# Optimization experiments

Measured on AMD Instinct MI355X. Metric: run time of the kernel, lower is better.

Reference implementation:

```python
import jax, jax.numpy as jnp
import numpy as np

B, NH, T, N, D = 4, 8, 2048, 512, 128
THETA = 2.0 ** 16
GAMMA = 0.995


def setup_inputs() -> dict:
    key = jax.random.key(0)
    kq, kv, ks = jax.random.split(key, 3)
    Q = jax.random.normal(kq, (B, NH, T, N), jnp.float32)
    V = jax.random.normal(kv, (B, NH, T, D), jnp.float32)
    S_prev = 0.01 * jax.random.normal(ks, (B, NH, N, D), jnp.float32)
    # get_freqs(N, theta=2**16): per-channel inverse frequencies
    freqs = jnp.asarray(1.0 / THETA ** (np.arange(N, dtype=np.float32) / N), jnp.float32)
    gamma = jnp.float32(GAMMA)
    return {"Q": Q, "V": V, "S_prev": S_prev, "freqs": freqs, "gamma": gamma}


def _rope(phases, v):
    """Rotary embedding with per-channel phases. phases broadcasts against v's
    last two dims (T, N); rotate-half formulation."""
    cos, sin = jnp.cos(phases), jnp.sin(phases)
    half = v.shape[-1] // 2
    v_rot = jnp.concatenate([-v[..., half:], v[..., :half]], axis=-1)
    return v * cos + v_rot * sin


def reference(Q, V, S_prev, freqs, gamma):
    # Q: (B,nh,T,N)  V: (B,nh,T,D)  S_prev: (B,nh,N,D)
    t_len = Q.shape[2]
    phases = jnp.arange(t_len, dtype=freqs.dtype)[:, None] * freqs[None, :]  # (T,N)
    QR = _rope(phases[None, None], Q)  # K == Q per the module's assert

    q_seq = jnp.moveaxis(QR, 2, 0)  # (T,B,nh,N)
    v_seq = jnp.moveaxis(V, 2, 0)   # (T,B,nh,D)

    def step(S, qv):
        q_t, v_t = qv
        out_t = jnp.einsum('bhn,bhnd->bhd', q_t, S)          # read before write
        S_new = (S + jnp.einsum('bhn,bhd->bhnd', q_t, v_t)) * gamma  # write + decay
        return S_new, out_t

    S_final, outs = jax.lax.scan(step, S_prev, (q_seq, v_seq))
    output = jnp.moveaxis(outs, 0, 2)  # (B,nh,T,D)
    return output, S_final
```

## Files before the change

kernel.cpp:

```cpp
#include <hip/hip_runtime.h>
#include <hip/hip_bf16.h>

typedef __attribute__((ext_vector_type(8))) short short8;
typedef __attribute__((ext_vector_type(4))) float f32x4;

#define MFMA16(a,b,c) __builtin_amdgcn_mfma_f32_16x16x32_bf16((a),(b),(c),0,0,0)

constexpr int BHn = 32;
constexpr int Tn  = 2048;
constexpr int Nn  = 512;
constexpr int Dn  = 128;
constexpr int CHn = 64;
constexpr int NCH = Tn / CHn;

static __device__ __forceinline__ unsigned short f2b(float x){
  __hip_bfloat16 h = __float2bfloat16(x);
  return *reinterpret_cast<unsigned short*>(&h);
}

__global__ __launch_bounds__(256) void rope_k(const float* __restrict__ Q,
                                              const float* __restrict__ freqs,
                                              unsigned short* __restrict__ QR){
  int gid = blockIdx.x * 256 + threadIdx.x;
  int np  = gid & 255;
  int t   = gid >> 8;
  float tf = (float)t;
  float f1 = freqs[np], f2 = freqs[np + 256];
  float s1, c1, s2, c2;
  sincosf(tf * f1, &s1, &c1);
  sincosf(tf * f2, &s2, &c2);
  size_t off = (size_t)t * Nn + np;
  for (int bh = 0; bh < BHn; ++bh){
    size_t base = (size_t)bh * Tn * Nn + off;
    float q1 = Q[base], q2 = Q[base + 256];
    QR[base]       = f2b(q1 * c1 - q2 * s1);
    QR[base + 256] = f2b(q2 * c2 + q1 * s2);
  }
}

__device__ __forceinline__ short8 ldfrag(const unsigned short* buf, int rowbase, int k0, int ld, int lane){
  int row = rowbase + (lane & 15);
  int col = (k0 + ((lane >> 4) << 3)) ^ ((row & 7) << 3);
  return *reinterpret_cast<const short8*>(buf + row * ld + col);
}
__device__ __forceinline__ short8 gfrag(const unsigned short* Qc, int rowbase, int k0, int lane){
  return *reinterpret_cast<const short8*>(
      Qc + (size_t)(rowbase + (lane & 15)) * Nn + k0 + ((lane >> 4) << 3));
}
__device__ __forceinline__ void stage_Rs(unsigned short* Rs, uint4 a, uint4 b, int dt, int n0){
  *reinterpret_cast<uint4*>(&Rs[ dt      * 512 + (n0 ^ (( dt      & 7) << 3))]) = a;
  *reinterpret_cast<uint4*>(&Rs[(dt + 1) * 512 + (n0 ^ (((dt + 1) & 7) << 3))]) = b;
}

__global__ __launch_bounds__(256) void pt_k(const unsigned short* __restrict__ QR,
                                            const float* __restrict__ gammap,
                                            unsigned short* __restrict__ Pt){
  __shared__ __align__(16) unsigned short Rs[64 * 512];
  __shared__ float gpow[65];
  const int tid = threadIdx.x, w = tid >> 6, lane = tid & 63;
  const int bh = blockIdx.x & 31, c = blockIdx.x >> 5;
  if (tid < 65) gpow[tid] = powf(gammap[0], (float)tid);
  const unsigned short* Qc = QR + (size_t)bh * Tn * Nn + (size_t)(c * CHn) * Nn;
  #pragma unroll
  for (int i = 0; i < 8; ++i){
    int p  = tid + i * 256;
    int dt = (p >> 6) << 1, n0 = (p & 63) << 3;
    const unsigned short* src = Qc + (size_t)dt * Nn + n0;
    uint4 a = *reinterpret_cast<const uint4*>(src);
    uint4 b = *reinterpret_cast<const uint4*>(src + Nn);
    stage_Rs(Rs, a, b, dt, n0);
  }
  __syncthreads();
  f32x4 p0 = {0.f,0.f,0.f,0.f}, p1 = p0, p2 = p0;
  for (int kb = 0; kb < 16; ++kb){
    int k0 = kb * 32;
    if (w == 0){
      short8 f0 = ldfrag(Rs,  0, k0, 512, lane);
      short8 f1 = ldfrag(Rs, 16, k0, 512, lane);
      p0 = MFMA16(f0, f0, p0);
      p1 = MFMA16(f1, f0, p1);
      p2 = MFMA16(f1, f1, p2);
    } else if (w == 1){
      short8 f0 = ldfrag(Rs,  0, k0, 512, lane);
      short8 f1 = ldfrag(Rs, 16, k0, 512, lane);
      short8 f2 = ldfrag(Rs, 32, k0, 512, lane);
      p0 = MFMA16(f2, f0, p0);
      p1 = MFMA16(f2, f1, p1);
      p2 = MFMA16(f2, f2, p2);
    } else if (w == 2){
      short8 f0 = ldfrag(Rs,  0, k0, 512, lane);
      short8 f1 = ldfrag(Rs, 16, k0, 512, lane);
      short8 f3 = ldfrag(Rs, 48, k0, 512, lane);
      p0 = MFMA16(f3, f0, p0);
      p1 = MFMA16(f3, f1, p1);
    } else {
      short8 f2 = ldfrag(Rs, 32, k0, 512, lane);
      short8 f3 = ldfrag(Rs, 48, k0, 512, lane);
      p0 = MFMA16(f3, f2, p0);
      p1 = MFMA16(f3, f3, p1);
    }
  }
  unsigned short* Pq = Pt + (size_t)(bh * NCH + c) * 4096;
  auto pwrite = [&](f32x4 pa, int tI, int tJ){
    int j  = tJ * 16 + (lane & 15);
    int i0 = tI * 16 + ((lane >> 4) << 2);
    #pragma unroll
    for (int r = 0; r < 4; ++r){
      int i = i0 + r;
      float v = (j < i) ? pa[r] * gpow[i] : 0.f;
      Pq[i * 64 + (j ^ ((i & 7) << 3))] = f2b(v);
    }
  };
  if      (w == 0){ pwrite(p0,0,0); pwrite(p1,1,0); pwrite(p2,1,1); pwrite(p0,0,1); }
  else if (w == 1){ pwrite(p0,2,0); pwrite(p1,2,1); pwrite(p2,2,2); pwrite(p0,0,2); }
  else if (w == 2){ pwrite(p0,3,0); pwrite(p1,3,1); pwrite(p0,0,3); pwrite(p1,1,2); }
  else            { pwrite(p0,3,2); pwrite(p1,3,3); pwrite(p0,1,3); pwrite(p1,2,3); }
}

__global__ __launch_bounds__(512, 1) void lattn_main(
    const unsigned short* __restrict__ QR,
    const unsigned short* __restrict__ Pt,
    const float* __restrict__ V,
    const float* __restrict__ S_prev,
    const float* __restrict__ gammap,
    float* __restrict__ Out,
    float* __restrict__ Sfin)
{
  __shared__ __align__(16) unsigned short SbTs[16 * 512];
  __shared__ __align__(16) unsigned short VTs[2][16 * 64];
  __shared__ float gpow[65], gpinv[65];

  const int tid  = threadIdx.x;
  const int w    = tid >> 6;
  const int lane = tid & 63;
  const int bh   = blockIdx.x & 31;
  const int dch  = blockIdx.x >> 5;
  const int d0   = dch * 16;
  const float g  = gammap[0];

  const unsigned short* QRbh = QR + (size_t)bh * Tn * Nn;
  const unsigned short* Ptbh = Pt + (size_t)bh * NCH * 4096;
  const float* Vbh = V + (size_t)bh * Tn * Dn;

  if (tid < 65){
    gpow[tid]  = powf(g,  (float)tid);
    gpinv[tid] = powf(g, -(float)tid);
  }

  const int snt = (w < 4) ? 2 : 6;
  const int sb  = (w < 4) ? w * 2 : 8 + (w - 4) * 6;
  f32x4 st[6];
  #pragma unroll
  for (int j = 0; j < 6; ++j) if (j < snt){
    int n = (sb + j) * 16 + (lane & 15);
    st[j] = *reinterpret_cast<const f32x4*>(
        S_prev + (size_t)bh * Nn * Dn + (size_t)n * Dn + d0 + ((lane >> 4) << 2));
  }
  __syncthreads();
  const float g64 = gpow[64];

  #pragma unroll
  for (int j = 0; j < 6; ++j) if (j < snt){
    int n  = (sb + j) * 16 + (lane & 15);
    int dl = (lane >> 4) << 2;
    #pragma unroll
    for (int r = 0; r < 4; ++r){
      int d = dl + r;
      SbTs[d * 512 + (n ^ ((d & 7) << 3))] = f2b(st[j][r]);
    }
  }
  {
    int dtv = tid >> 3, dp = (tid & 7) << 1;
    const float* vp = Vbh + (size_t)dtv * Dn + d0 + dp;
    float sc = gpinv[dtv];
    VTs[0][ dp      * 64 + (dtv ^ (( dp      & 7) << 3))] = f2b(vp[0] * sc);
    VTs[0][(dp + 1) * 64 + (dtv ^ (((dp + 1) & 7) << 3))] = f2b(vp[1] * sc);
  }
  __syncthreads();

  for (int c = 0; c < NCH; ++c){
    const int t0 = c * CHn;
    const int vb = c & 1;
    const bool pf = (c + 1 < NCH);
    const unsigned short* Qc = QRbh + (size_t)t0 * Nn;

    float va0 = 0.f, va1 = 0.f;
    const int dtv_ = tid >> 3;
    if (pf){
      const float* vp = Vbh + (size_t)(t0 + CHn + dtv_) * Dn + d0 + ((tid & 7) << 1);
      va0 = vp[0]; va1 = vp[1];
    }

    if (w < 4){
      f32x4 oacc = {0.f, 0.f, 0.f, 0.f};
      for (int kb = 0; kb < 16; ++kb){
        int k0 = kb * 32;
        short8 fs = ldfrag(SbTs, 0, k0, 512, lane);
        short8 fi = gfrag(Qc, w * 16, k0, lane);
        oacc = MFMA16(fs, fi, oacc);
      }
      float gi = gpow[w * 16 + (lane & 15)];
      #pragma unroll
      for (int r = 0; r < 4; ++r) oacc[r] *= gi;
      const unsigned short* Pq = Ptbh + (size_t)c * 4096;
      #pragma unroll
      for (int ks = 0; ks < 2; ++ks){
        short8 av = ldfrag(VTs[vb], 0, ks * 32, 64, lane);
        short8 bp = ldfrag(Pq, w * 16, ks * 32, 64, lane);
        oacc = MFMA16(av, bp, oacc);
      }
      int ti = t0 + w * 16 + (lane & 15);
      *reinterpret_cast<f32x4*>(
          Out + (size_t)bh * Tn * Dn + (size_t)ti * Dn + d0 + ((lane >> 4) << 2)) = oacc;
    }
    #pragma unroll
    for (int ks = 0; ks < 2; ++ks){
      short8 av = ldfrag(VTs[vb], 0, ks * 32, 64, lane);
      #pragma unroll
      for (int j = 0; j < 6; ++j) if (j < snt){
        int n = (sb + j) * 16 + (lane & 15);
        const unsigned short* col = Qc + (size_t)(ks * 32 + ((lane >> 4) << 3)) * Nn + n;
        short8 bn;
        #pragma unroll
        for (int e = 0; e < 8; ++e) bn[e] = (short)col[(size_t)e * Nn];
        st[j] = MFMA16(av, bn, st[j]);
      }
    }
    #pragma unroll
    for (int j = 0; j < 6; ++j) if (j < snt)
      #pragma unroll
      for (int r = 0; r < 4; ++r) st[j][r] *= g64;
    __syncthreads();

    #pragma unroll
    for (int j = 0; j < 6; ++j) if (j < snt){
      int n  = (sb + j) * 16 + (lane & 15);
      int dl = (lane >> 4) << 2;
      #pragma unroll
      for (int r = 0; r < 4; ++r){
        int d = dl + r;
        SbTs[d * 512 + (n ^ ((d & 7) << 3))] = f2b(st[j][r]);
      }
    }
    if (pf){
      int dp = (tid & 7) << 1;
      float sc = gpinv[dtv_];
      VTs[vb ^ 1][ dp      * 64 + (dtv_ ^ (( dp      & 7) << 3))] = f2b(va0 * sc);
      VTs[vb ^ 1][(dp + 1) * 64 + (dtv_ ^ (((dp + 1) & 7) << 3))] = f2b(va1 * sc);
    }
    __syncthreads();
  }

  #pragma unroll
  for (int j = 0; j < 6; ++j) if (j < snt){
    int n = (sb + j) * 16 + (lane & 15);
    *reinterpret_cast<f32x4*>(
        Sfin + (size_t)bh * Nn * Dn + (size_t)n * Dn + d0 + ((lane >> 4) << 2)) = st[j];
  }
}

extern "C" void kernel_launch(void* const* d_in, const int* in_sizes, int n_in,
                              void* d_out, int out_size, void* d_ws, size_t ws_size,
                              hipStream_t stream){
  const float* Q      = (const float*)d_in[0];
  const float* V      = (const float*)d_in[1];
  const float* S_prev = (const float*)d_in[2];
  const float* freqs  = (const float*)d_in[3];
  const float* gamma  = (const float*)d_in[4];
  float* Out  = (float*)d_out;
  float* Sfin = Out + (size_t)BHn * Tn * Dn;
  unsigned short* QR = (unsigned short*)d_ws;
  unsigned short* Pt = QR + (size_t)BHn * Tn * Nn;

  rope_k<<<2048, 256, 0, stream>>>(Q, freqs, QR);
  pt_k<<<1024, 256, 0, stream>>>(QR, gamma, Pt);
  lattn_main<<<256, 512, 0, stream>>>(QR, Pt, V, S_prev, gamma, Out, Sfin);
}
```

Baseline: 225.0 us.

## Double chunk length to 128 and add off-diagonal intra-chunk P kernel

Raises the chunk size of the chunked linear-attention recurrence from 64 to 128, halving the number of sequential state-update iterations and barriers in the main kernel. The intra-chunk P matrix becomes 128x128. It is built from two diagonal 64-blocks by the existing pt_k and a new po_k kernel for the off-diagonal block. V staging now uses vectorized float4 loads. The trade-off is more intra-chunk work and larger decay exponents (gamma^-127 scaling in bf16), which may affect accuracy.

```diff
diff --git a/kernel.cpp b/kernel.cpp
--- a/kernel.cpp
+++ b/kernel.cpp
@@ -10,7 +10,7 @@
 constexpr int Tn  = 2048;
 constexpr int Nn  = 512;
 constexpr int Dn  = 128;
-constexpr int CHn = 64;
+constexpr int CHn = 128;
 constexpr int NCH = Tn / CHn;
 
 static __device__ __forceinline__ unsigned short f2b(float x){
@@ -56,11 +56,12 @@
                                             const float* __restrict__ gammap,
                                             unsigned short* __restrict__ Pt){
   __shared__ __align__(16) unsigned short Rs[64 * 512];
-  __shared__ float gpow[65];
+  __shared__ float gpow[129];
   const int tid = threadIdx.x, w = tid >> 6, lane = tid & 63;
-  const int bh = blockIdx.x & 31, c = blockIdx.x >> 5;
-  if (tid < 65) gpow[tid] = powf(gammap[0], (float)tid);
-  const unsigned short* Qc = QR + (size_t)bh * Tn * Nn + (size_t)(c * CHn) * Nn;
+  const int bh = blockIdx.x & 31, cc = (blockIdx.x >> 5) & 15, sub = blockIdx.x >> 9;
+  const int ro = sub * 64;
+  if (tid < 129) gpow[tid] = powf(gammap[0], (float)tid);
+  const unsigned short* Qc = QR + (size_t)bh * Tn * Nn + (size_t)(cc * CHn + ro) * Nn;
   #pragma unroll
   for (int i = 0; i < 8; ++i){
     int p  = tid + i * 256;
@@ -100,21 +101,55 @@
       p1 = MFMA16(f3, f3, p1);
     }
   }
-  unsigned short* Pq = Pt + (size_t)(bh * NCH + c) * 4096;
+  unsigned short* Pq = Pt + (size_t)(bh * NCH + cc) * (CHn * CHn);
   auto pwrite = [&](f32x4 pa, int tI, int tJ){
     int j  = tJ * 16 + (lane & 15);
     int i0 = tI * 16 + ((lane >> 4) << 2);
     #pragma unroll
     for (int r = 0; r < 4; ++r){
       int i = i0 + r;
-      float v = (j < i) ? pa[r] * gpow[i] : 0.f;
-      Pq[i * 64 + (j ^ ((i & 7) << 3))] = f2b(v);
+      float v = (j < i) ? pa[r] * gpow[i + ro] : 0.f;
+      Pq[(i + ro) * CHn + ro + (j ^ ((i & 7) << 3))] = f2b(v);
     }
   };
   if      (w == 0){ pwrite(p0,0,0); pwrite(p1,1,0); pwrite(p2,1,1); pwrite(p0,0,1); }
   else if (w == 1){ pwrite(p0,2,0); pwrite(p1,2,1); pwrite(p2,2,2); pwrite(p0,0,2); }
   else if (w == 2){ pwrite(p0,3,0); pwrite(p1,3,1); pwrite(p0,0,3); pwrite(p1,1,2); }
   else            { pwrite(p0,3,2); pwrite(p1,3,3); pwrite(p0,1,3); pwrite(p1,2,3); }
+}
+
+__global__ __launch_bounds__(256) void po_k(const unsigned short* __restrict__ QR,
+                                            const float* __restrict__ gammap,
+                                            unsigned short* __restrict__ Pt){
+  __shared__ float gpow[129];
+  const int tid = threadIdx.x, w = tid >> 6, lane = tid & 63;
+  const int bh = blockIdx.x & 31, cc = blockIdx.x >> 5;
+  if (tid < 129) gpow[tid] = powf(gammap[0], (float)tid);
+  __syncthreads();
+  const unsigned short* QB = QR + (size_t)bh * Tn * Nn + (size_t)(cc * CHn) * Nn;
+  const unsigned short* QA = QB + (size_t)64 * Nn;
+  f32x4 acc[4] = {{0.f,0.f,0.f,0.f},{0.f,0.f,0.f,0.f},{0.f,0.f,0.f,0.f},{0.f,0.f,0.f,0.f}};
+  for (int kb = 0; kb < 16; ++kb){
+    int k0 = kb * 32;
+    short8 fa = gfrag(QA, w * 16, k0, lane);
+    #pragma unroll
+    for (int t = 0; t < 4; ++t){
+      short8 fb = gfrag(QB, t * 16, k0, lane);
+      acc[t] = MFMA16(fa, fb, acc[t]);
+    }
+  }
+  unsigned short* Pq = Pt + (size_t)(bh * NCH + cc) * (CHn * CHn);
+  #pragma unroll
+  for (int t = 0; t < 4; ++t){
+    int j  = t * 16 + (lane & 15);
+    int i0 = w * 16 + ((lane >> 4) << 2);
+    #pragma unroll
+    for (int r = 0; r < 4; ++r){
+      int i = i0 + r;
+      float v = acc[t][r] * gpow[64 + i];
+      Pq[(64 + i) * CHn + (j ^ ((i & 7) << 3))] = f2b(v);
+    }
+  }
 }
 
 __global__ __launch_bounds__(512, 1) void lattn_main(
@@ -127,8 +162,8 @@
     float* __restrict__ Sfin)
 {
   __shared__ __align__(16) unsigned short SbTs[16 * 512];
-  __shared__ __align__(16) unsigned short VTs[2][16 * 64];
-  __shared__ float gpow[65], gpinv[65];
+  __shared__ __align__(16) unsigned short VTs[2][16 * 128];
+  __shared__ float gpow[129], gpinv[129];
 
   const int tid  = threadIdx.x;
   const int w    = tid >> 6;
@@ -139,10 +174,10 @@
   const float g  = gammap[0];
 
   const unsigned short* QRbh = QR + (size_t)bh * Tn * Nn;
-  const unsigned short* Ptbh = Pt + (size_t)bh * NCH * 4096;
+  const unsigned short* Ptbh = Pt + (size_t)bh * NCH * (CHn * CHn);
   const float* Vbh = V + (size_t)bh * Tn * Dn;
 
-  if (tid < 65){
+  if (tid < 129){
     gpow[tid]  = powf(g,  (float)tid);
     gpinv[tid] = powf(g, -(float)tid);
   }
@@ -157,7 +192,7 @@
         S_prev + (size_t)bh * Nn * Dn + (size_t)n * Dn + d0 + ((lane >> 4) << 2));
   }
   __syncthreads();
-  const float g64 = gpow[64];
+  const float g128 = gpow[128];
 
   #pragma unroll
   for (int j = 0; j < 6; ++j) if (j < snt){
@@ -170,11 +205,14 @@
     }
   }
   {
-    int dtv = tid >> 3, dp = (tid & 7) << 1;
-    const float* vp = Vbh + (size_t)dtv * Dn + d0 + dp;
+    int dtv = tid >> 2, dp0 = (tid & 3) << 2;
+    f32x4 v4 = *reinterpret_cast<const f32x4*>(Vbh + (size_t)dtv * Dn + d0 + dp0);
     float sc = gpinv[dtv];
-    VTs[0][ dp      * 64 + (dtv ^ (( dp      & 7) << 3))] = f2b(vp[0] * sc);
-    VTs[0][(dp + 1) * 64 + (dtv ^ (((dp + 1) & 7) << 3))] = f2b(vp[1] * sc);
+    #pragma unroll
+    for (int r = 0; r < 4; ++r){
+      int d = dp0 + r;
+      VTs[0][d * 128 + (dtv ^ ((d & 7) << 3))] = f2b(v4[r] * sc);
+    }
   }
   __syncthreads();
 
@@ -184,38 +222,47 @@
     const bool pf = (c + 1 < NCH);
     const unsigned short* Qc = QRbh + (size_t)t0 * Nn;
 
-    float va0 = 0.f, va1 = 0.f;
-    const int dtv_ = tid >> 3;
-    if (pf){
-      const float* vp = Vbh + (size_t)(t0 + CHn + dtv_) * Dn + d0 + ((tid & 7) << 1);
-      va0 = vp[0]; va1 = vp[1];
-    }
+    f32x4 va4 = {0.f, 0.f, 0.f, 0.f};
+    const int dtv_ = tid >> 2, dp0_ = (tid & 3) << 2;
+    if (pf)
+      va4 = *reinterpret_cast<const f32x4*>(Vbh + (size_t)(t0 + CHn + dtv_) * Dn + d0 + dp0_);
 
     if (w < 4){
-      f32x4 oacc = {0.f, 0.f, 0.f, 0.f};
+      const int it0 = w, it1 = w + 4;
+      f32x4 o0 = {0.f,0.f,0.f,0.f}, o1 = o0;
       for (int kb = 0; kb < 16; ++kb){
         int k0 = kb * 32;
         short8 fs = ldfrag(SbTs, 0, k0, 512, lane);
-        short8 fi = gfrag(Qc, w * 16, k0, lane);
-        oacc = MFMA16(fs, fi, oacc);
-      }
-      float gi = gpow[w * 16 + (lane & 15)];
-      #pragma unroll
-      for (int r = 0; r < 4; ++r) oacc[r] *= gi;
-      const unsigned short* Pq = Ptbh + (size_t)c * 4096;
-      #pragma unroll
-      for (int ks = 0; ks < 2; ++ks){
-        short8 av = ldfrag(VTs[vb], 0, ks * 32, 64, lane);
-        short8 bp = ldfrag(Pq, w * 16, ks * 32, 64, lane);
-        oacc = MFMA16(av, bp, oacc);
-      }
-      int ti = t0 + w * 16 + (lane & 15);
+        short8 fa = gfrag(Qc, it0 * 16, k0, lane);
+        short8 fb = gfrag(Qc, it1 * 16, k0, lane);
+        o0 = MFMA16(fs, fa, o0);
+        o1 = MFMA16(fs, fb, o1);
+      }
+      float g0 = gpow[it0 * 16 + (lane & 15)];
+      float g1 = gpow[it1 * 16 + (lane & 15)];
+      #pragma unroll
+      for (int r = 0; r < 4; ++r){ o0[r] *= g0; o1[r] *= g1; }
+      const unsigned short* Pq = Ptbh + (size_t)c * (CHn * CHn);
+      #pragma unroll
+      for (int ks = 0; ks < 4; ++ks){
+        short8 av = ldfrag(VTs[vb], 0, ks * 32, 128, lane);
+        if (ks < 2){
+          short8 b0 = ldfrag(Pq, it0 * 16, ks * 32, CHn, lane);
+          o0 = MFMA16(av, b0, o0);
+        }
+        short8 b1 = ldfrag(Pq, it1 * 16, ks * 32, CHn, lane);
+        o1 = MFMA16(av, b1, o1);
+      }
+      int ti0 = t0 + it0 * 16 + (lane & 15);
+      int ti1 = t0 + it1 * 16 + (lane & 15);
       *reinterpret_cast<f32x4*>(
-          Out + (size_t)bh * Tn * Dn + (size_t)ti * Dn + d0 + ((lane >> 4) << 2)) = oacc;
-    }
-    #pragma unroll
-    for (int ks = 0; ks < 2; ++ks){
-      short8 av = ldfrag(VTs[vb], 0, ks * 32, 64, lane);
+          Out + (size_t)bh * Tn * Dn + (size_t)ti0 * Dn + d0 + ((lane >> 4) << 2)) = o0;
+      *reinterpret_cast<f32x4*>(
+          Out + (size_t)bh * Tn * Dn + (size_t)ti1 * Dn + d0 + ((lane >> 4) << 2)) = o1;
+    }
+    #pragma unroll
+    for (int ks = 0; ks < 4; ++ks){
+      short8 av = ldfrag(VTs[vb], 0, ks * 32, 128, lane);
       #pragma unroll
       for (int j = 0; j < 6; ++j) if (j < snt){
         int n = (sb + j) * 16 + (lane & 15);
@@ -229,7 +276,7 @@
     #pragma unroll
     for (int j = 0; j < 6; ++j) if (j < snt)
       #pragma unroll
-      for (int r = 0; r < 4; ++r) st[j][r] *= g64;
+      for (int r = 0; r < 4; ++r) st[j][r] *= g128;
     __syncthreads();
 
     #pragma unroll
@@ -243,10 +290,12 @@
       }
     }
     if (pf){
-      int dp = (tid & 7) << 1;
       float sc = gpinv[dtv_];
-      VTs[vb ^ 1][ dp      * 64 + (dtv_ ^ (( dp      & 7) << 3))] = f2b(va0 * sc);
-      VTs[vb ^ 1][(dp + 1) * 64 + (dtv_ ^ (((dp + 1) & 7) << 3))] = f2b(va1 * sc);
+      #pragma unroll
+      for (int r = 0; r < 4; ++r){
+        int d = dp0_ + r;
+        VTs[vb ^ 1][d * 128 + (dtv_ ^ ((d & 7) << 3))] = f2b(va4[r] * sc);
+      }
     }
     __syncthreads();
   }
@@ -274,5 +323,6 @@
 
   rope_k<<<2048, 256, 0, stream>>>(Q, freqs, QR);
   pt_k<<<1024, 256, 0, stream>>>(QR, gamma, Pt);
+  po_k<<<512, 256, 0, stream>>>(QR, gamma, Pt);
   lattn_main<<<256, 512, 0, stream>>>(QR, Pt, V, S_prev, gamma, Out, Sfin);
 }
```

New measurement: 219.6 us. 2.4% less time.
